# Optimization experiments

Measured on AMD Instinct MI355X. Metric: run time of the kernel, lower is better.

Reference implementation:

```python
import jax, jax.numpy as jnp
import numpy as np

B = 8          # batch
S = 256        # nx+1 = ny+1 grid resolution
N = S * S      # number of DoFs per component
DIM = 2        # output vector dimension (= d_out)
W = 32         # FNO channel width
M1 = 12        # Fourier modes dim 1
M2 = 12        # Fourier modes dim 2
WF = 128       # final MLP hidden width
NL = 4         # number of Fourier layers
PADF = 8       # padding fraction denominator


def setup_inputs() -> dict:
    key = jax.random.key(0)
    ks = jax.random.split(key, 16)
    sc = 1.0 / (W * W)  # torch FNO spectral weight init scale
    return {
        "x": jax.random.normal(ks[0], (B, N), jnp.float32),
        "d2v_in": jax.random.permutation(ks[1], jnp.arange(N)),
        "v2d_out": jax.random.permutation(ks[2], jnp.arange(N)),
        "fc0_w": jax.random.normal(ks[3], (W, 3), jnp.float32) * 0.1,
        "fc0_b": jnp.zeros((W,), jnp.float32),
        "spec_w1r": jax.random.uniform(ks[4], (NL, W, W, M1, M2), jnp.float32) * sc,
        "spec_w1i": jax.random.uniform(ks[5], (NL, W, W, M1, M2), jnp.float32) * sc,
        "spec_w2r": jax.random.uniform(ks[6], (NL, W, W, M1, M2), jnp.float32) * sc,
        "spec_w2i": jax.random.uniform(ks[7], (NL, W, W, M1, M2), jnp.float32) * sc,
        "conv_w": jax.random.normal(ks[8], (NL, W, W), jnp.float32) * 0.05,
        "conv_b": jnp.zeros((NL, W), jnp.float32),
        "mlp_w1": jax.random.normal(ks[9], (WF, W), jnp.float32) * 0.05,
        "mlp_b1": jnp.zeros((WF,), jnp.float32),
        "mlp_w2": jax.random.normal(ks[10], (DIM, WF), jnp.float32) * 0.05,
        "mlp_b2": jnp.zeros((DIM,), jnp.float32),
    }


def _speconv(x, w1, w2):
    # x: (B, C, H, Wd) real; w1/w2: (C_in, C_out, M1, M2) complex64
    Bh, C, H, Wd = x.shape
    xft = jnp.fft.rfft2(x)  # (B, C, H, Wd//2+1)
    o1 = jnp.einsum('bixy,ioxy->boxy', xft[:, :, :M1, :M2], w1)
    o2 = jnp.einsum('bixy,ioxy->boxy', xft[:, :, -M1:, :M2], w2)
    out_ft = jnp.zeros((Bh, C, H, Wd // 2 + 1), jnp.complex64)
    out_ft = out_ft.at[:, :, :M1, :M2].set(o1).at[:, :, -M1:, :M2].set(o2)
    return jnp.fft.irfft2(out_ft, s=(H, Wd))


def reference(x, d2v_in, v2d_out, fc0_w, fc0_b,
              spec_w1r, spec_w1i, spec_w2r, spec_w2i,
              conv_w, conv_b, mlp_w1, mlp_b1, mlp_w2, mlp_b2):
    # DoF -> vertex gather and lift to image
    xg = x[:, d2v_in].reshape(B, 1, S, S)
    h = jnp.transpose(xg, (0, 2, 3, 1))  # (B, S, S, 1)
    # append normalized grid coordinates (get_grid2d)
    g = jnp.linspace(0.0, 1.0, S, dtype=jnp.float32)
    grid = jnp.stack(jnp.meshgrid(g, g, indexing='ij'), axis=-1)  # (S, S, 2)
    grid = jnp.broadcast_to(grid[None], (B, S, S, 2))
    h = jnp.concatenate([h, grid], axis=-1)
    # fc0 lifting
    h = h @ fc0_w.T + fc0_b              # (B, S, S, W)
    h = jnp.transpose(h, (0, 3, 1, 2))   # (B, W, S, S)
    # zero pad (non-periodic domain)
    p = S // PADF
    h = jnp.pad(h, ((0, 0), (0, 0), (0, p), (0, p)))  # (B, W, S+p, S+p)
    w1 = (spec_w1r + 1j * spec_w1i).astype(jnp.complex64)
    w2 = (spec_w2r + 1j * spec_w2i).astype(jnp.complex64)
    for l in range(NL):
        sp = _speconv(h, w1[l], w2[l])
        cv = jnp.einsum('bchw,oc->bohw', h, conv_w[l]) + conv_b[l][None, :, None, None]
        h = cv + sp
        if l != NL - 1:
            h = jax.nn.gelu(h, approximate=False)  # torch GELU default = exact erf
    # crop padding (s_outputspace=None path)
    h = h[..., :S, :S]
    # final two-layer MLP projection
    h = jnp.transpose(h, (0, 2, 3, 1))  # (B, S, S, W)
    h = jax.nn.gelu(h @ mlp_w1.T + mlp_b1, approximate=False) @ mlp_w2.T + mlp_b2
    h = jnp.transpose(h, (0, 3, 1, 2)).reshape(B, DIM, -1)  # (B, DIM, N)
    # vertex -> DoF scatter/gather and interleave components
    out = h[:, :, v2d_out]              # (B, DIM, N)
    out = jnp.transpose(out, (0, 2, 1)).reshape(B, -1)  # (B, N*DIM)
    return out
```

## Files before the change

### kernel.cpp

```cpp
#include <hip/hip_runtime.h>
#include <math.h>

#define S    256
#define Hp   288
#define C    32
#define KY   12
#define NK   24
#define Bn   8
#define PI_D 3.14159265358979323846264338327950288

#define SZ_TW  (NK*Hp*2)
#define OFF_TW 0
#define OFF_TWT (OFF_TW + SZ_TW)
#define SZ_TWT (Hp*KY*2)
#define OFF_H  (OFF_TWT + SZ_TWT)
#define SZ_H   (Bn*C*Hp*Hp)
#define OFF_Y  (OFF_H + SZ_H)
#define SZ_Y   (Bn*C*Hp*KY*2)
#define OFF_X  (OFF_Y + SZ_Y)
#define SZ_X   (Bn*C*NK*KY*2)
#define OFF_O  (OFF_X + 2*SZ_X)
#define SZ_O   SZ_X
#define OFF_Z  (OFF_O + SZ_O)
#define SZ_Z   (Bn*Hp*C*KY*2)
#define OFF_T  (OFF_Z + SZ_Z)
#define SZ_T   (Bn*S*S*2)

#define GELU(v) (0.5f*(v)*(1.0f+erff((v)*0.70710678118654752f)))
#define SCHED_FENCE() __builtin_amdgcn_sched_barrier(0)

__global__ void k_tw(float* __restrict__ tw, float* __restrict__ twT) {
    int i = blockIdx.x * 256 + threadIdx.x;
    if (i >= NK * Hp) return;
    int k = i / Hp, xx = i % Hp;
    int f = (k < KY) ? k : (k + 264);
    int m = (f * xx) % Hp;
    double th = (2.0 * PI_D * (double)m) / (double)Hp;
    float c = (float)cos(th), s = (float)sin(th);
    tw[2 * i] = c; tw[2 * i + 1] = s;
    if (k < KY) { twT[xx * 24 + 2 * k] = c; twT[xx * 24 + 2 * k + 1] = s; }
}

__global__ __launch_bounds__(256, 1) void k_embed(
        const float* __restrict__ xin, const int* __restrict__ d2v,
        const float* __restrict__ fw, const float* __restrict__ fb,
        const float* __restrict__ twT, float* __restrict__ h, float* __restrict__ Y) {
    __shared__ __align__(16) float xs[256];
    __shared__ __align__(16) float YP[3072];
    int x = blockIdx.x, b = blockIdx.y, tid = threadIdx.x;
    size_t rowbase = (size_t)b * 2654208 + (size_t)x * 288;
    if (x >= S) {
        for (int i = tid; i < 32 * 72; i += 256) {
            int c = i / 72, q = i % 72;
            *(float4*)&h[rowbase + (size_t)c * 82944 + q * 4] = make_float4(0, 0, 0, 0);
        }
        for (int i = tid; i < 768; i += 256)
            Y[((size_t)(b * 32 + i / 24) * 288 + x) * 24 + (i % 24)] = 0.f;
        return;
    }
    xs[tid] = xin[b * 65536 + d2v[x * 256 + tid]];
    int o = tid & 31, g = tid >> 5;
    float w0 = fw[o * 3], w1 = fw[o * 3 + 1], w2 = fw[o * 3 + 2], bb = fb[o];
    float gx = x * (1.0f / 255.0f);
    __syncthreads();
    float pr[12], pi[12];
    #pragma unroll
    for (int k = 0; k < 12; ++k) { pr[k] = 0.f; pi[k] = 0.f; }
    #pragma unroll 1
    for (int c3 = 0; c3 < 3; ++c3) {
        int ybase = g * 36 + c3 * 12;
        float acc[12];
        #pragma unroll
        for (int j = 0; j < 12; ++j) {
            int y = ybase + j;
            acc[j] = (y < S) ? (w0 * xs[y < S ? y : 0] + w1 * gx + w2 * (y * (1.0f / 255.0f)) + bb) : 0.f;
        }
        float* hw = h + rowbase + (size_t)o * 82944 + ybase;
        #pragma unroll
        for (int q = 0; q < 3; ++q)
            *(float4*)&hw[4 * q] = make_float4(acc[4*q], acc[4*q+1], acc[4*q+2], acc[4*q+3]);
        SCHED_FENCE();
        #pragma unroll
        for (int jp = 0; jp < 6; ++jp) {
            #pragma unroll
            for (int u = 0; u < 2; ++u) {
                int j = jp * 2 + u;
                int y = ybase + j;
                const float* tg = twT + y * 24;
                float tc[24];
                #pragma unroll
                for (int q = 0; q < 6; ++q) *(float4*)&tc[4 * q] = *(const float4*)&tg[4 * q];
                float v = acc[j];
                #pragma unroll
                for (int k = 0; k < 12; ++k) { pr[k] += v * tc[2 * k]; pi[k] -= v * tc[2 * k + 1]; }
            }
            SCHED_FENCE();
        }
    }
    #pragma unroll
    for (int k = 0; k < 12; ++k) { pr[k] += __shfl_xor(pr[k], 32); pi[k] += __shfl_xor(pi[k], 32); }
    if ((tid & 32) == 0) {
        float* dst = YP + ((tid >> 6) * 32 + o) * 24;
        #pragma unroll
        for (int k = 0; k < 12; ++k) { dst[2 * k] = pr[k]; dst[2 * k + 1] = pi[k]; }
    }
    __syncthreads();
    for (int i = tid; i < 768; i += 256) {
        float s = YP[i] + YP[768 + i] + YP[1536 + i] + YP[2304 + i];
        Y[((size_t)(b * 32 + i / 24) * 288 + x) * 24 + (i % 24)] = s;
    }
}

__global__ __launch_bounds__(288) void k_dftx(const float* __restrict__ Y,
                                              const float* __restrict__ tw,
                                              float* __restrict__ X) {
    __shared__ __align__(16) float Ys[144 * 24];
    int c = blockIdx.x, b = blockIdx.y, half = blockIdx.z, tid = threadIdx.x;
    const float* Yb = Y + (size_t)(b * 32 + c) * 6912 + half * 3456;
    for (int i = tid; i < 864; i += 288)
        *(float4*)&Ys[4 * i] = *(const float4*)&Yb[4 * i];
    __syncthreads();
    int k = tid / 12, ky = tid % 12;
    const float* twk = tw + k * 576 + half * 288;
    float xr = 0.f, xi = 0.f;
    #pragma unroll 4
    for (int xx = 0; xx < 144; ++xx) {
        float yr = Ys[xx * 24 + 2 * ky], yi = Ys[xx * 24 + 2 * ky + 1];
        float cc = twk[2 * xx], ss = twk[2 * xx + 1];
        xr += yr * cc + yi * ss;
        xi += yi * cc - yr * ss;
    }
    size_t oo = (size_t)half * SZ_X + ((size_t)(b * 32 + c) * 288 + tid) * 2;
    X[oo] = xr; X[oo + 1] = xi;
}

__global__ void k_spec(const float* __restrict__ X,
                       const float* __restrict__ w1r, const float* __restrict__ w1i,
                       const float* __restrict__ w2r, const float* __restrict__ w2i,
                       float* __restrict__ O, int l) {
    int t = blockIdx.x * 256 + threadIdx.x;
    int ky = t % KY; int k = (t / KY) % NK; int o = (t / (NK * KY)) % C; int b = t / (C * NK * KY);
    int kk = (k < KY) ? k : (k - KY);
    const float* wr = (k < KY) ? w1r : w2r;
    const float* wi = (k < KY) ? w1i : w2i;
    size_t wbase = (size_t)l * C * C * 144 + (size_t)o * 144 + kk * 12 + ky;
    size_t xbase = (size_t)b * C * NK * KY * 2 + (k * KY + ky) * 2;
    float ar = 0.f, ai = 0.f;
    #pragma unroll 8
    for (int i = 0; i < C; ++i) {
        size_t xo = xbase + (size_t)i * NK * KY * 2;
        float xr = X[xo]     + X[SZ_X + xo];
        float xi = X[xo + 1] + X[SZ_X + xo + 1];
        float wrr = wr[wbase + (size_t)i * C * 144];
        float wii = wi[wbase + (size_t)i * C * 144];
        ar += xr * wrr - xi * wii;
        ai += xr * wii + xi * wrr;
    }
    size_t oo = (((size_t)b * C + o) * NK * KY + k * KY + ky) * 2;
    O[oo] = ar; O[oo + 1] = ai;
}

__global__ __launch_bounds__(384) void k_idftx(const float* __restrict__ O,
                                               const float* __restrict__ tw,
                                               float* __restrict__ Z) {
    int x0 = blockIdx.x * 32; int c = blockIdx.y, b = blockIdx.z;
    int row = threadIdx.x & 31, ky = threadIdx.x >> 5;
    int x = x0 + row;
    const float* Ob = O + ((size_t)(b * C + c)) * NK * KY * 2 + ky * 2;
    float zr = 0.f, zi = 0.f;
    #pragma unroll
    for (int k = 0; k < NK; ++k) {
        float orr = Ob[k * KY * 2], oii = Ob[k * KY * 2 + 1];
        float cc = tw[(k * Hp + x) * 2], ss = tw[(k * Hp + x) * 2 + 1];
        zr += orr * cc - oii * ss;
        zi += orr * ss + oii * cc;
    }
    size_t o = ((((size_t)b * Hp + x) * C + c) * KY + ky) * 2;
    Z[o] = zr; Z[o + 1] = zi;
}

__global__ __launch_bounds__(256, 1) void k_conv(
        float* __restrict__ h, const float* __restrict__ Z,
        const float* __restrict__ cw, const float* __restrict__ cb,
        const float* __restrict__ twT, float* __restrict__ Y,
        int l, int flags) {
    __shared__ __align__(16) float hs[32 * 288];
    __shared__ __align__(16) float YP[3072];
    __shared__ __align__(16) float cws[32 * 33];
    __shared__ float cbs[32];
    int x = blockIdx.x, b = blockIdx.y, tid = threadIdx.x;
    size_t rowbase = (size_t)b * 2654208 + (size_t)x * 288;
    const float* hb = h + rowbase;
    for (int i = tid; i < 32 * 72; i += 256)
        *(float4*)&hs[4 * i] = *(const float4*)&hb[(size_t)(i / 72) * 82944 + (i % 72) * 4];
    for (int i = tid; i < 32 * 32; i += 256)
        cws[(i >> 5) * 33 + (i & 31)] = cw[l * 1024 + i];
    if (tid < 32) cbs[tid] = cb[l * 32 + tid];
    int o = tid & 31, g = tid >> 5;
    const float* Zr = Z + ((size_t)(b * 288 + x) * 32 + o) * 24;
    float zr[12], zi[12];
    #pragma unroll
    for (int q = 0; q < 6; ++q) {
        float4 zv = *(const float4*)&Zr[4 * q];
        zr[2*q] = zv.x; zi[2*q] = zv.y; zr[2*q+1] = zv.z; zi[2*q+1] = zv.w;
    }
    __syncthreads();
    float bias = cbs[o];
    float pr[12], pi[12];
    #pragma unroll
    for (int k = 0; k < 12; ++k) { pr[k] = 0.f; pi[k] = 0.f; }
    const int gelu_f = flags & 1, wy = flags & 2;
    #pragma unroll 1
    for (int c3 = 0; c3 < 3; ++c3) {
        int ybase = g * 36 + c3 * 12;
        float acc[12];
        #pragma unroll
        for (int j = 0; j < 12; ++j) acc[j] = bias;
        #pragma unroll 8
        for (int c = 0; c < 32; ++c) {
            float w = cws[o * 33 + c];
            const float* hr = &hs[c * 288 + ybase];
            float4 h0 = *(const float4*)&hr[0];
            float4 h1 = *(const float4*)&hr[4];
            float4 h2 = *(const float4*)&hr[8];
            acc[0] += h0.x * w; acc[1] += h0.y * w; acc[2]  += h0.z * w; acc[3]  += h0.w * w;
            acc[4] += h1.x * w; acc[5] += h1.y * w; acc[6]  += h1.z * w; acc[7]  += h1.w * w;
            acc[8] += h2.x * w; acc[9] += h2.y * w; acc[10] += h2.z * w; acc[11] += h2.w * w;
        }
        SCHED_FENCE();
        #pragma unroll
        for (int jp = 0; jp < 6; ++jp) {
            #pragma unroll
            for (int u = 0; u < 2; ++u) {
                int j = jp * 2 + u;
                int y = ybase + j;
                const float* tg = twT + y * 24;
                float tc[24];
                #pragma unroll
                for (int q = 0; q < 6; ++q) *(float4*)&tc[4 * q] = *(const float4*)&tg[4 * q];
                float sp = zr[0] * tc[0] - zi[0] * tc[1];
                #pragma unroll
                for (int k = 1; k < 12; ++k) sp += 2.f * (zr[k] * tc[2*k] - zi[k] * tc[2*k+1]);
                float val = acc[j] + sp * (1.0f / 82944.0f);
                if (gelu_f) val = GELU(val);
                acc[j] = val;
                if (wy) {
                    #pragma unroll
                    for (int k = 0; k < 12; ++k) { pr[k] += val * tc[2*k]; pi[k] -= val * tc[2*k+1]; }
                }
            }
            SCHED_FENCE();
        }
        float* hw = h + rowbase + (size_t)o * 82944 + ybase;
        #pragma unroll
        for (int q = 0; q < 3; ++q)
            *(float4*)&hw[4 * q] = make_float4(acc[4*q], acc[4*q+1], acc[4*q+2], acc[4*q+3]);
        SCHED_FENCE();
    }
    if (wy) {
        #pragma unroll
        for (int k = 0; k < 12; ++k) { pr[k] += __shfl_xor(pr[k], 32); pi[k] += __shfl_xor(pi[k], 32); }
        if ((tid & 32) == 0) {
            float* dst = YP + ((tid >> 6) * 32 + o) * 24;
            #pragma unroll
            for (int k = 0; k < 12; ++k) { dst[2 * k] = pr[k]; dst[2 * k + 1] = pi[k]; }
        }
        __syncthreads();
        for (int i = tid; i < 768; i += 256) {
            float s = YP[i] + YP[768 + i] + YP[1536 + i] + YP[2304 + i];
            Y[((size_t)(b * 32 + i / 24) * 288 + x) * 24 + (i % 24)] = s;
        }
    }
}

__global__ __launch_bounds__(256) void k_mlp(const float* __restrict__ h,
                                             const float* __restrict__ w1, const float* __restrict__ b1,
                                             const float* __restrict__ w2, const float* __restrict__ b2,
                                             float* __restrict__ tmp) {
    int bid = blockIdx.x;
    int b = bid >> 7;
    int x = ((bid & 127) << 1) + (threadIdx.x >> 7);
    int lane = threadIdx.x & 127;
    const float* hb = h + (size_t)b * 2654208 + (size_t)x * 288;
    float hc0[32], hc1[32];
    #pragma unroll
    for (int c = 0; c < 32; ++c) {
        hc0[c] = hb[(size_t)c * 82944 + lane];
        hc1[c] = hb[(size_t)c * 82944 + lane + 128];
    }
    float o00 = 0.f, o01 = 0.f, o10 = 0.f, o11 = 0.f;
    for (int f = 0; f < 128; ++f) {
        float a0 = b1[f], a1 = a0;
        #pragma unroll
        for (int c = 0; c < 32; ++c) {
            float w = w1[f * 32 + c];
            a0 += hc0[c] * w; a1 += hc1[c] * w;
        }
        float wa = w2[f], wb = w2[128 + f];
        float g0 = GELU(a0), g1 = GELU(a1);
        o00 += g0 * wa; o01 += g0 * wb;
        o10 += g1 * wa; o11 += g1 * wb;
    }
    float bb0 = b2[0], bb1 = b2[1];
    int p0 = x * 256 + lane;
    size_t base = (size_t)b * 65536;
    *(float2*)&tmp[(base + p0) * 2]       = make_float2(o00 + bb0, o01 + bb1);
    *(float2*)&tmp[(base + p0 + 128) * 2] = make_float2(o10 + bb0, o11 + bb1);
}

__global__ void k_scatter(const float* __restrict__ tmp, const int* __restrict__ v2d,
                          float* __restrict__ out) {
    int id = blockIdx.x * 256 + threadIdx.x;
    int b = id >> 16; int j = id & 65535;
    int p = v2d[j];
    const float2 v = *(const float2*)(tmp + ((size_t)(b << 16) + p) * 2);
    *(float2*)(out + (size_t)id * 2) = v;
}

extern "C" void kernel_launch(void* const* d_in, const int* in_sizes, int n_in,
                              void* d_out, int out_size, void* d_ws, size_t ws_size,
                              hipStream_t stream) {
    const float* xin   = (const float*)d_in[0];
    const int*   d2v   = (const int*)  d_in[1];
    const int*   v2d   = (const int*)  d_in[2];
    const float* fc0w  = (const float*)d_in[3];
    const float* fc0b  = (const float*)d_in[4];
    const float* w1r   = (const float*)d_in[5];
    const float* w1i   = (const float*)d_in[6];
    const float* w2r   = (const float*)d_in[7];
    const float* w2i   = (const float*)d_in[8];
    const float* cw    = (const float*)d_in[9];
    const float* cb    = (const float*)d_in[10];
    const float* mw1   = (const float*)d_in[11];
    const float* mb1   = (const float*)d_in[12];
    const float* mw2   = (const float*)d_in[13];
    const float* mb2   = (const float*)d_in[14];

    float* ws  = (float*)d_ws;
    float* TW  = ws + OFF_TW;
    float* TWT = ws + OFF_TWT;
    float* H   = ws + OFF_H;
    float* Y   = ws + OFF_Y;
    float* X   = ws + OFF_X;
    float* O   = ws + OFF_O;
    float* Z   = ws + OFF_Z;
    float* T   = ws + OFF_T;

    k_tw<<<(NK * Hp + 255) / 256, 256, 0, stream>>>(TW, TWT);
    k_embed<<<dim3(Hp, Bn), 256, 0, stream>>>(xin, d2v, fc0w, fc0b, TWT, H, Y);

    for (int l = 0; l < 4; ++l) {
        k_dftx<<<dim3(32, Bn, 2), 288, 0, stream>>>(Y, TW, X);
        k_spec<<<(Bn * C * NK * KY) / 256, 256, 0, stream>>>(X, w1r, w1i, w2r, w2i, O, l);
        k_idftx<<<dim3(9, 32, Bn), 384, 0, stream>>>(O, TW, Z);
        k_conv<<<dim3(Hp, Bn), 256, 0, stream>>>(H, Z, cw, cb, TWT, Y, l, (l != 3) ? 3 : 0);
    }

    k_mlp<<<1024, 256, 0, stream>>>(H, mw1, mb1, mw2, mb2, T);
    k_scatter<<<(Bn * S * S) / 256, 256, 0, stream>>>(T, v2d, (float*)d_out);
}
```

Measured before the change: 866.7 us.

## Stage half-period twiddles in LDS and split conv row into two passes

```diff
diff --git a/kernel.cpp b/kernel.cpp
--- a/kernel.cpp
+++ b/kernel.cpp
@@ -41,11 +41,35 @@
     if (k < KY) { twT[xx * 24 + 2 * k] = c; twT[xx * 24 + 2 * k + 1] = s; }
 }
 
+template<bool HI>
+__device__ __forceinline__ void fdft12(const float* __restrict__ twh, int rb,
+                                       const float* acc, float* pr, float* pi) {
+    #pragma unroll
+    for (int jp = 0; jp < 6; ++jp) {
+        #pragma unroll
+        for (int u = 0; u < 2; ++u) {
+            int j = jp * 2 + u;
+            const float* tg = twh + (rb + j) * 24;
+            float tc[24];
+            #pragma unroll
+            for (int q = 0; q < 6; ++q) *(float4*)&tc[4 * q] = *(const float4*)&tg[4 * q];
+            float v = acc[j];
+            #pragma unroll
+            for (int k = 0; k < 12; ++k) {
+                float vk = (HI && (k & 1)) ? -v : v;
+                pr[k] += vk * tc[2 * k]; pi[k] -= vk * tc[2 * k + 1];
+            }
+        }
+        SCHED_FENCE();
+    }
+}
+
 __global__ __launch_bounds__(256, 1) void k_embed(
         const float* __restrict__ xin, const int* __restrict__ d2v,
         const float* __restrict__ fw, const float* __restrict__ fb,
         const float* __restrict__ twT, float* __restrict__ h, float* __restrict__ Y) {
     __shared__ __align__(16) float xs[256];
+    __shared__ __align__(16) float twh[144 * 24];
     __shared__ __align__(16) float YP[3072];
     int x = blockIdx.x, b = blockIdx.y, tid = threadIdx.x;
     size_t rowbase = (size_t)b * 2654208 + (size_t)x * 288;
@@ -58,6 +82,8 @@
             Y[((size_t)(b * 32 + i / 24) * 288 + x) * 24 + (i % 24)] = 0.f;
         return;
     }
+    for (int i = tid; i < 864; i += 256)
+        *(float4*)&twh[4 * i] = *(const float4*)&twT[4 * i];
     xs[tid] = xin[b * 65536 + d2v[x * 256 + tid]];
     int o = tid & 31, g = tid >> 5;
     float w0 = fw[o * 3], w1 = fw[o * 3 + 1], w2 = fw[o * 3 + 2], bb = fb[o];
@@ -80,22 +106,9 @@
         for (int q = 0; q < 3; ++q)
             *(float4*)&hw[4 * q] = make_float4(acc[4*q], acc[4*q+1], acc[4*q+2], acc[4*q+3]);
         SCHED_FENCE();
-        #pragma unroll
-        for (int jp = 0; jp < 6; ++jp) {
-            #pragma unroll
-            for (int u = 0; u < 2; ++u) {
-                int j = jp * 2 + u;
-                int y = ybase + j;
-                const float* tg = twT + y * 24;
-                float tc[24];
-                #pragma unroll
-                for (int q = 0; q < 6; ++q) *(float4*)&tc[4 * q] = *(const float4*)&tg[4 * q];
-                float v = acc[j];
-                #pragma unroll
-                for (int k = 0; k < 12; ++k) { pr[k] += v * tc[2 * k]; pi[k] -= v * tc[2 * k + 1]; }
-            }
-            SCHED_FENCE();
-        }
+        int rb = (g & 3) * 36 + c3 * 12;
+        if (g < 4) fdft12<false>(twh, rb, acc, pr, pi);
+        else       fdft12<true >(twh, rb, acc, pr, pi);
     }
     #pragma unroll
     for (int k = 0; k < 12; ++k) { pr[k] += __shfl_xor(pr[k], 32); pi[k] += __shfl_xor(pi[k], 32); }
@@ -179,24 +192,57 @@
     Z[o] = zr; Z[o + 1] = zi;
 }
 
+template<bool HI>
+__device__ __forceinline__ void epi6(const float* __restrict__ twh, int rb,
+                                     float* acc, const float* zr, const float* zi,
+                                     float* pr, float* pi, int gelu_f, int wy) {
+    #pragma unroll
+    for (int jp = 0; jp < 3; ++jp) {
+        #pragma unroll
+        for (int u = 0; u < 2; ++u) {
+            int j = jp * 2 + u;
+            const float* tg = twh + (rb + j) * 24;
+            float tc[24];
+            #pragma unroll
+            for (int q = 0; q < 6; ++q) *(float4*)&tc[4 * q] = *(const float4*)&tg[4 * q];
+            float t0 = zr[0] * tc[0] - zi[0] * tc[1];
+            float sE = 0.f, sO = 0.f;
+            #pragma unroll
+            for (int k = 1; k < 12; ++k) {
+                float t = zr[k] * tc[2 * k] - zi[k] * tc[2 * k + 1];
+                if (k & 1) sO += t; else sE += t;
+            }
+            float sp = HI ? (t0 + 2.f * (sE - sO)) : (t0 + 2.f * (sE + sO));
+            float val = acc[j] + sp * (1.0f / 82944.0f);
+            if (gelu_f) val = GELU(val);
+            acc[j] = val;
+            if (wy) {
+                #pragma unroll
+                for (int k = 0; k < 12; ++k) {
+                    float vk = (HI && (k & 1)) ? -val : val;
+                    pr[k] += vk * tc[2 * k]; pi[k] -= vk * tc[2 * k + 1];
+                }
+            }
+        }
+        SCHED_FENCE();
+    }
+}
+
 __global__ __launch_bounds__(256, 1) void k_conv(
         float* __restrict__ h, const float* __restrict__ Z,
         const float* __restrict__ cw, const float* __restrict__ cb,
         const float* __restrict__ twT, float* __restrict__ Y,
         int l, int flags) {
-    __shared__ __align__(16) float hs[32 * 288];
-    __shared__ __align__(16) float YP[3072];
-    __shared__ __align__(16) float cws[32 * 33];
-    __shared__ float cbs[32];
+    __shared__ __align__(16) float smem[32 * 144];
+    __shared__ __align__(16) float twh[144 * 24];
+    __shared__ __align__(16) float cwsT[1024];
     int x = blockIdx.x, b = blockIdx.y, tid = threadIdx.x;
+    int o = tid & 31, g = tid >> 5;
     size_t rowbase = (size_t)b * 2654208 + (size_t)x * 288;
-    const float* hb = h + rowbase;
-    for (int i = tid; i < 32 * 72; i += 256)
-        *(float4*)&hs[4 * i] = *(const float4*)&hb[(size_t)(i / 72) * 82944 + (i % 72) * 4];
-    for (int i = tid; i < 32 * 32; i += 256)
-        cws[(i >> 5) * 33 + (i & 31)] = cw[l * 1024 + i];
-    if (tid < 32) cbs[tid] = cb[l * 32 + tid];
-    int o = tid & 31, g = tid >> 5;
+    for (int i = tid; i < 864; i += 256)
+        *(float4*)&twh[4 * i] = *(const float4*)&twT[4 * i];
+    for (int i = tid; i < 1024; i += 256)
+        cwsT[i] = cw[l * 1024 + (i & 31) * 32 + (i >> 5)];
     const float* Zr = Z + ((size_t)(b * 288 + x) * 32 + o) * 24;
     float zr[12], zi[12];
     #pragma unroll
@@ -204,62 +250,49 @@
         float4 zv = *(const float4*)&Zr[4 * q];
         zr[2*q] = zv.x; zi[2*q] = zv.y; zr[2*q+1] = zv.z; zi[2*q+1] = zv.w;
     }
-    __syncthreads();
-    float bias = cbs[o];
+    float bias = cb[l * 32 + o];
     float pr[12], pi[12];
     #pragma unroll
     for (int k = 0; k < 12; ++k) { pr[k] = 0.f; pi[k] = 0.f; }
     const int gelu_f = flags & 1, wy = flags & 2;
     #pragma unroll 1
-    for (int c3 = 0; c3 < 3; ++c3) {
-        int ybase = g * 36 + c3 * 12;
-        float acc[12];
-        #pragma unroll
-        for (int j = 0; j < 12; ++j) acc[j] = bias;
-        #pragma unroll 8
-        for (int c = 0; c < 32; ++c) {
-            float w = cws[o * 33 + c];
-            const float* hr = &hs[c * 288 + ybase];
-            float4 h0 = *(const float4*)&hr[0];
-            float4 h1 = *(const float4*)&hr[4];
-            float4 h2 = *(const float4*)&hr[8];
-            acc[0] += h0.x * w; acc[1] += h0.y * w; acc[2]  += h0.z * w; acc[3]  += h0.w * w;
-            acc[4] += h1.x * w; acc[5] += h1.y * w; acc[6]  += h1.z * w; acc[7]  += h1.w * w;
-            acc[8] += h2.x * w; acc[9] += h2.y * w; acc[10] += h2.z * w; acc[11] += h2.w * w;
-        }
-        SCHED_FENCE();
-        #pragma unroll
-        for (int jp = 0; jp < 6; ++jp) {
-            #pragma unroll
-            for (int u = 0; u < 2; ++u) {
-                int j = jp * 2 + u;
-                int y = ybase + j;
-                const float* tg = twT + y * 24;
-                float tc[24];
-                #pragma unroll
-                for (int q = 0; q < 6; ++q) *(float4*)&tc[4 * q] = *(const float4*)&tg[4 * q];
-                float sp = zr[0] * tc[0] - zi[0] * tc[1];
-                #pragma unroll
-                for (int k = 1; k < 12; ++k) sp += 2.f * (zr[k] * tc[2*k] - zi[k] * tc[2*k+1]);
-                float val = acc[j] + sp * (1.0f / 82944.0f);
-                if (gelu_f) val = GELU(val);
-                acc[j] = val;
-                if (wy) {
-                    #pragma unroll
-                    for (int k = 0; k < 12; ++k) { pr[k] += val * tc[2*k]; pi[k] -= val * tc[2*k+1]; }
-                }
+    for (int pass = 0; pass < 2; ++pass) {
+        __syncthreads();
+        const float* hsrc = h + rowbase + pass * 144;
+        for (int i = tid; i < 1152; i += 256)
+            *(float4*)&smem[4 * i] = *(const float4*)&hsrc[(size_t)(i / 36) * 82944 + (i % 36) * 4];
+        __syncthreads();
+        #pragma unroll 1
+        for (int p = 0; p < 3; ++p) {
+            int rb = g * 18 + 6 * p;
+            float acc[6];
+            #pragma unroll
+            for (int j = 0; j < 6; ++j) acc[j] = bias;
+            #pragma unroll 8
+            for (int c = 0; c < 32; ++c) {
+                float w = cwsT[c * 32 + o];
+                const float* hr = &smem[c * 144 + rb];
+                float2 a0 = *(const float2*)&hr[0];
+                float2 a1 = *(const float2*)&hr[2];
+                float2 a2 = *(const float2*)&hr[4];
+                acc[0] += a0.x * w; acc[1] += a0.y * w; acc[2] += a1.x * w;
+                acc[3] += a1.y * w; acc[4] += a2.x * w; acc[5] += a2.y * w;
             }
             SCHED_FENCE();
-        }
-        float* hw = h + rowbase + (size_t)o * 82944 + ybase;
-        #pragma unroll
-        for (int q = 0; q < 3; ++q)
-            *(float4*)&hw[4 * q] = make_float4(acc[4*q], acc[4*q+1], acc[4*q+2], acc[4*q+3]);
-        SCHED_FENCE();
+            if (pass == 0) epi6<false>(twh, rb, acc, zr, zi, pr, pi, gelu_f, wy);
+            else           epi6<true >(twh, rb, acc, zr, zi, pr, pi, gelu_f, wy);
+            float* hw = h + rowbase + (size_t)o * 82944 + pass * 144 + rb;
+            *(float2*)&hw[0] = make_float2(acc[0], acc[1]);
+            *(float2*)&hw[2] = make_float2(acc[2], acc[3]);
+            *(float2*)&hw[4] = make_float2(acc[4], acc[5]);
+            SCHED_FENCE();
+        }
     }
     if (wy) {
         #pragma unroll
         for (int k = 0; k < 12; ++k) { pr[k] += __shfl_xor(pr[k], 32); pi[k] += __shfl_xor(pi[k], 32); }
+        __syncthreads();
+        float* YP = smem;
         if ((tid & 32) == 0) {
             float* dst = YP + ((tid >> 6) * 32 + o) * 24;
             #pragma unroll
```

Measured after the change: 899.7 us. 3.8% more time.

## Stage twiddles in LDS, exploit quarter-period symmetry in embed, pad conv tile

Applied to the files above, without the earlier changes.

```diff
diff --git a/kernel.cpp b/kernel.cpp
--- a/kernel.cpp
+++ b/kernel.cpp
@@ -41,11 +41,59 @@
     if (k < KY) { twT[xx * 24 + 2 * k] = c; twT[xx * 24 + 2 * k + 1] = s; }
 }
 
+template<int Q>
+__device__ __forceinline__ void embed_body(
+        const float* __restrict__ xs, const float* __restrict__ twq,
+        float* __restrict__ h, size_t rowbase, int o, int g,
+        float w0, float w1, float w2, float bb, float gx,
+        float* pr, float* pi) {
+    #pragma unroll 1
+    for (int c3 = 0; c3 < 3; ++c3) {
+        int ybase = g * 36 + c3 * 12;
+        int rowq  = (g & 1) * 36 + c3 * 12;
+        float acc[12];
+        #pragma unroll
+        for (int j = 0; j < 12; ++j) {
+            int y = ybase + j;
+            acc[j] = (y < S) ? (w0 * xs[y < S ? y : 0] + w1 * gx + w2 * (y * (1.0f / 255.0f)) + bb) : 0.f;
+        }
+        float* hw = h + rowbase + (size_t)o * 82944 + ybase;
+        #pragma unroll
+        for (int q = 0; q < 3; ++q)
+            *(float4*)&hw[4 * q] = make_float4(acc[4*q], acc[4*q+1], acc[4*q+2], acc[4*q+3]);
+        SCHED_FENCE();
+        #pragma unroll
+        for (int jp = 0; jp < 6; ++jp) {
+            #pragma unroll
+            for (int u = 0; u < 2; ++u) {
+                int j = jp * 2 + u;
+                const float* tg = twq + (rowq + j) * 24;
+                float tc[24];
+                #pragma unroll
+                for (int q = 0; q < 6; ++q) *(float4*)&tc[4 * q] = *(const float4*)&tg[4 * q];
+                float v = acc[j];
+                pr[0] += v;
+                #pragma unroll
+                for (int k = 1; k < 12; ++k) {
+                    const int e = (k * Q) & 3;
+                    float c = tc[2 * k], s = tc[2 * k + 1];
+                    if      (e == 0) { pr[k] += v * c; pi[k] -= v * s; }
+                    else if (e == 1) { pr[k] -= v * s; pi[k] -= v * c; }
+                    else if (e == 2) { pr[k] -= v * c; pi[k] += v * s; }
+                    else             { pr[k] += v * s; pi[k] += v * c; }
+                }
+            }
+            SCHED_FENCE();
+        }
+    }
+}
+
 __global__ __launch_bounds__(256, 1) void k_embed(
         const float* __restrict__ xin, const int* __restrict__ d2v,
         const float* __restrict__ fw, const float* __restrict__ fb,
         const float* __restrict__ twT, float* __restrict__ h, float* __restrict__ Y) {
     __shared__ __align__(16) float xs[256];
+    __shared__ __align__(16) float twq[1728];
     __shared__ __align__(16) float YP[3072];
     int x = blockIdx.x, b = blockIdx.y, tid = threadIdx.x;
     size_t rowbase = (size_t)b * 2654208 + (size_t)x * 288;
@@ -58,6 +106,8 @@
             Y[((size_t)(b * 32 + i / 24) * 288 + x) * 24 + (i % 24)] = 0.f;
         return;
     }
+    for (int i = tid; i < 432; i += 256)
+        *(float4*)&twq[4 * i] = *(const float4*)&twT[4 * i];
     xs[tid] = xin[b * 65536 + d2v[x * 256 + tid]];
     int o = tid & 31, g = tid >> 5;
     float w0 = fw[o * 3], w1 = fw[o * 3 + 1], w2 = fw[o * 3 + 2], bb = fb[o];
@@ -66,36 +116,11 @@
     float pr[12], pi[12];
     #pragma unroll
     for (int k = 0; k < 12; ++k) { pr[k] = 0.f; pi[k] = 0.f; }
-    #pragma unroll 1
-    for (int c3 = 0; c3 < 3; ++c3) {
-        int ybase = g * 36 + c3 * 12;
-        float acc[12];
-        #pragma unroll
-        for (int j = 0; j < 12; ++j) {
-            int y = ybase + j;
-            acc[j] = (y < S) ? (w0 * xs[y < S ? y : 0] + w1 * gx + w2 * (y * (1.0f / 255.0f)) + bb) : 0.f;
-        }
-        float* hw = h + rowbase + (size_t)o * 82944 + ybase;
-        #pragma unroll
-        for (int q = 0; q < 3; ++q)
-            *(float4*)&hw[4 * q] = make_float4(acc[4*q], acc[4*q+1], acc[4*q+2], acc[4*q+3]);
-        SCHED_FENCE();
-        #pragma unroll
-        for (int jp = 0; jp < 6; ++jp) {
-            #pragma unroll
-            for (int u = 0; u < 2; ++u) {
-                int j = jp * 2 + u;
-                int y = ybase + j;
-                const float* tg = twT + y * 24;
-                float tc[24];
-                #pragma unroll
-                for (int q = 0; q < 6; ++q) *(float4*)&tc[4 * q] = *(const float4*)&tg[4 * q];
-                float v = acc[j];
-                #pragma unroll
-                for (int k = 0; k < 12; ++k) { pr[k] += v * tc[2 * k]; pi[k] -= v * tc[2 * k + 1]; }
-            }
-            SCHED_FENCE();
-        }
+    switch (tid >> 6) {
+        case 0: embed_body<0>(xs, twq, h, rowbase, o, g, w0, w1, w2, bb, gx, pr, pi); break;
+        case 1: embed_body<1>(xs, twq, h, rowbase, o, g, w0, w1, w2, bb, gx, pr, pi); break;
+        case 2: embed_body<2>(xs, twq, h, rowbase, o, g, w0, w1, w2, bb, gx, pr, pi); break;
+        default: embed_body<3>(xs, twq, h, rowbase, o, g, w0, w1, w2, bb, gx, pr, pi); break;
     }
     #pragma unroll
     for (int k = 0; k < 12; ++k) { pr[k] += __shfl_xor(pr[k], 32); pi[k] += __shfl_xor(pi[k], 32); }
@@ -184,15 +209,19 @@
         const float* __restrict__ cw, const float* __restrict__ cb,
         const float* __restrict__ twT, float* __restrict__ Y,
         int l, int flags) {
-    __shared__ __align__(16) float hs[32 * 288];
-    __shared__ __align__(16) float YP[3072];
+    __shared__ __align__(16) float hs[32 * 292];
+    __shared__ __align__(16) float twy[288 * 24];
     __shared__ __align__(16) float cws[32 * 33];
     __shared__ float cbs[32];
     int x = blockIdx.x, b = blockIdx.y, tid = threadIdx.x;
     size_t rowbase = (size_t)b * 2654208 + (size_t)x * 288;
     const float* hb = h + rowbase;
-    for (int i = tid; i < 32 * 72; i += 256)
-        *(float4*)&hs[4 * i] = *(const float4*)&hb[(size_t)(i / 72) * 82944 + (i % 72) * 4];
+    for (int i = tid; i < 32 * 72; i += 256) {
+        int c = i / 72, q = i % 72;
+        *(float4*)&hs[c * 292 + q * 4] = *(const float4*)&hb[(size_t)c * 82944 + q * 4];
+    }
+    for (int i = tid; i < 1728; i += 256)
+        *(float4*)&twy[4 * i] = *(const float4*)&twT[4 * i];
     for (int i = tid; i < 32 * 32; i += 256)
         cws[(i >> 5) * 33 + (i & 31)] = cw[l * 1024 + i];
     if (tid < 32) cbs[tid] = cb[l * 32 + tid];
@@ -219,7 +248,7 @@
         #pragma unroll 8
         for (int c = 0; c < 32; ++c) {
             float w = cws[o * 33 + c];
-            const float* hr = &hs[c * 288 + ybase];
+            const float* hr = &hs[c * 292 + ybase];
             float4 h0 = *(const float4*)&hr[0];
             float4 h1 = *(const float4*)&hr[4];
             float4 h2 = *(const float4*)&hr[8];
@@ -234,10 +263,9 @@
             for (int u = 0; u < 2; ++u) {
                 int j = jp * 2 + u;
                 int y = ybase + j;
-                const float* tg = twT + y * 24;
                 float tc[24];
                 #pragma unroll
-                for (int q = 0; q < 6; ++q) *(float4*)&tc[4 * q] = *(const float4*)&tg[4 * q];
+                for (int q = 0; q < 6; ++q) *(float4*)&tc[4 * q] = *(const float4*)&twy[y * 24 + 4 * q];
                 float sp = zr[0] * tc[0] - zi[0] * tc[1];
                 #pragma unroll
                 for (int k = 1; k < 12; ++k) sp += 2.f * (zr[k] * tc[2*k] - zi[k] * tc[2*k+1]);
@@ -260,6 +288,8 @@
     if (wy) {
         #pragma unroll
         for (int k = 0; k < 12; ++k) { pr[k] += __shfl_xor(pr[k], 32); pi[k] += __shfl_xor(pi[k], 32); }
+        __syncthreads();
+        float* YP = twy;
         if ((tid & 32) == 0) {
             float* dst = YP + ((tid >> 6) * 32 + o) * 24;
             #pragma unroll
```

Result: faster. 820.3 us (-5.4%).
